# Kernel optimization log

Measured on AMD Instinct MI355X. Metric: run time of the kernel, lower is better.

The kernel has to match this reference:

```python
import jax, jax.numpy as jnp
import numpy as np
import math

B, H, W = 8, 256, 256
CIN, COUT, K = 64, 64, 3
STYLE_IN = 512  # latent dim fed into EqualLinear
LIN_SCALE = 1.0 / math.sqrt(STYLE_IN)        # EqualLinear scale (lr_mul=1)
CONV_SCALE = 1.0 / math.sqrt(CIN * K * K)    # ModulatedConv2D scale


def setup_inputs() -> dict:
    key = jax.random.key(0)
    k1, k2, k3, k4 = jax.random.split(key, 4)
    inputs = jax.random.normal(k1, (B, H, W, CIN), dtype=jnp.float32)
    style = jax.random.normal(k2, (B, STYLE_IN), dtype=jnp.float32)
    # EqualLinear params: weight ~ N(0,1), bias init = 1
    mod_weight = jax.random.normal(k3, (STYLE_IN, CIN), dtype=jnp.float32)
    mod_bias = jnp.ones((CIN,), dtype=jnp.float32)
    # Conv weight [1, out_channel, in_channel, k, k] ~ N(0,1)
    weight = jax.random.normal(k4, (1, COUT, CIN, K, K), dtype=jnp.float32)
    return {"inputs": inputs, "style": style, "mod_weight": mod_weight,
            "mod_bias": mod_bias, "weight": weight}


def _per_sample_conv(xb, wb):
    # xb: [H, W, Cin]; wb: [Cout, Cin, K, K]
    w_hwio = jnp.transpose(wb, (2, 3, 1, 0))  # [K, K, Cin, Cout]
    y = jax.lax.conv_general_dilated(
        xb[None], w_hwio, window_strides=(1, 1), padding="SAME",
        dimension_numbers=("NHWC", "HWIO", "NHWC"))
    return y[0]


def reference(inputs, style, mod_weight, mod_bias, weight):
    # EqualLinear modulation: s = style @ (W * scale) + bias  -> [B, Cin]
    s = style @ (mod_weight * LIN_SCALE) + mod_bias
    # Modulate: [B, Cout, Cin, K, K]
    w = CONV_SCALE * weight * s[:, None, :, None, None]
    # Demodulate over (Cin, K, K)
    demod = jax.lax.rsqrt(jnp.sum(jnp.square(w), axis=(2, 3, 4)) + 1e-8)
    w = w * demod[:, :, None, None, None]
    # Grouped conv (groups = batch) == per-sample conv, vmapped over batch
    out = jax.vmap(_per_sample_conv)(inputs, w)  # [B, H, W, Cout]
    return out
```

## Files before the change

kernel.cpp:

```cpp
#include <hip/hip_runtime.h>

#define BATCH 8
#define HH 256
#define WW 256
#define CI 64
#define CO 64
#define STYLE_IN 512

typedef __bf16 bf16x8 __attribute__((ext_vector_type(8)));
typedef float  f32x4  __attribute__((ext_vector_type(4)));
typedef unsigned short u16x8 __attribute__((ext_vector_type(8)));

static __device__ inline unsigned short f2bf(float f) {
    union { float f; unsigned int u; } a; a.f = f;
    unsigned int u = a.u;
    u += 0x7fffu + ((u >> 16) & 1u);
    return (unsigned short)(u >> 16);
}

__global__ __launch_bounds__(256) void modulate_kernel(
    const float* __restrict__ style, const float* __restrict__ mod_weight,
    const float* __restrict__ mod_bias, const float* __restrict__ weight,
    unsigned short* __restrict__ wbf)
{
    const int b = blockIdx.x;
    const int t = threadIdx.x;
    __shared__ float sp[4][64];
    __shared__ float s_mod[64];
    __shared__ float dpart[64][4];
    __shared__ float demod[64];

    const float LIN_SCALE  = 0.044194173824159216f;
    const float CONV_SCALE = 0.041666666666666664f;

    {
        const int ci = t & 63, part = t >> 6;
        float acc = 0.f;
        const float* st = style + b * STYLE_IN + part * 128;
        const float* mw = mod_weight + part * 128 * 64 + ci;
        #pragma unroll 8
        for (int j = 0; j < 128; ++j) acc += st[j] * mw[j * 64];
        sp[part][ci] = acc;
    }
    __syncthreads();
    if (t < 64)
        s_mod[t] = (sp[0][t] + sp[1][t] + sp[2][t] + sp[3][t]) * LIN_SCALE + mod_bias[t];
    __syncthreads();

    {
        const int co = t >> 2, part = t & 3;
        float acc = 0.f;
        const float* wp = weight + co * 576 + part * 144;
        #pragma unroll
        for (int ci2 = 0; ci2 < 16; ++ci2) {
            float s = s_mod[part * 16 + ci2];
            #pragma unroll
            for (int tp = 0; tp < 9; ++tp) {
                float v = wp[ci2 * 9 + tp] * s;
                acc += v * v;
            }
        }
        dpart[co][part] = acc * (CONV_SCALE * CONV_SCALE);
    }
    __syncthreads();
    if (t < 64)
        demod[t] = rsqrtf(dpart[t][0] + dpart[t][1] + dpart[t][2] + dpart[t][3] + 1e-8f);
    __syncthreads();

    for (int i = t; i < 9 * 64 * 64; i += 256) {
        int ci  = i & 63;
        int co  = (i >> 6) & 63;
        int tap = i >> 12;
        float v = CONV_SCALE * weight[co * 576 + ci * 9 + tap] * s_mod[ci] * demod[co];
        wbf[((b * 9 + tap) * 64 + co) * 64 + ci] = f2bf(v);
    }
}

#define PXS 72
#define ROWPX 130
#define ROW_ELEMS (ROWPX * PXS)

__global__ __launch_bounds__(256, 2) void conv_kernel(
    const float* __restrict__ x, const unsigned short* __restrict__ wbf,
    float* __restrict__ out)
{
    __shared__ unsigned short xs[4 * ROW_ELEMS];

    const int tid = threadIdx.x;
    const int x0  = blockIdx.x * 128;
    const int y0  = blockIdx.y * 8;
    const int b   = blockIdx.z;

    auto issue = [&](int yin, f32x4* v) {
        const bool rok = (unsigned)yin < (unsigned)HH;
        const float* src = x + ((size_t)(b * HH + (rok ? yin : 0))) * WW * CI;
        #pragma unroll
        for (int k = 0; k < 5; ++k) {
            int i  = tid + k * 256;
            int px = i >> 3, cg = i & 7;
            int xin = x0 - 1 + px;
            bool ok = rok && ((unsigned)xin < (unsigned)WW) && (i < 1040);
            const float* p = src + (size_t)xin * CI + cg * 8;
            f32x4 z = {0.f, 0.f, 0.f, 0.f};
            v[2 * k]     = ok ? *(const f32x4*)p       : z;
            v[2 * k + 1] = ok ? *(const f32x4*)(p + 4) : z;
        }
    };
    auto commit = [&](int slot, const f32x4* v) {
        unsigned short* dst = xs + slot * ROW_ELEMS;
        #pragma unroll
        for (int k = 0; k < 5; ++k) {
            int i = tid + k * 256;
            if (k == 4 && i >= 1040) continue;
            int px = i >> 3, cg = i & 7;
            u16x8 u;
            #pragma unroll
            for (int e = 0; e < 4; ++e) {
                u[e]     = f2bf(v[2 * k][e]);
                u[e + 4] = f2bf(v[2 * k + 1][e]);
            }
            *(u16x8*)&dst[px * PXS + cg * 8] = u;
        }
    };

    {
        f32x4 v[10];
        issue(y0 - 1, v); commit(0, v);
        issue(y0,     v); commit(1, v);
        issue(y0 + 1, v); commit(2, v);
    }

    const int wave = tid >> 6, lane = tid & 63;
    const int lm = lane & 15, lq = lane >> 4;
    const int wr = wave >> 1;
    const int wc = wave & 1;
    const int p0 = wr * 64;

    bf16x8 wreg[9][2][2];
    {
        const unsigned short* wl = wbf + (size_t)b * 9 * 4096
                                 + (size_t)(wc * 32 + lm) * 64 + lq * 8;
        #pragma unroll
        for (int tap = 0; tap < 9; ++tap)
            #pragma unroll
            for (int ni = 0; ni < 2; ++ni)
                #pragma unroll
                for (int ks = 0; ks < 2; ++ks)
                    wreg[tap][ni][ks] =
                        *(const bf16x8*)(wl + tap * 4096 + ni * 1024 + ks * 32);
    }

    __syncthreads();

    const int aoff_lane = (p0 + lm) * PXS + lq * 8;

    f32x4 vbuf[10];
    issue(y0 + 2, vbuf);

    #pragma unroll
    for (int j = 0; j < 8; ++j) {
        const int y = y0 + j;

        f32x4 acc[4][2];
        #pragma unroll
        for (int mi = 0; mi < 4; ++mi)
            #pragma unroll
            for (int ni = 0; ni < 2; ++ni)
                acc[mi][ni] = (f32x4){0.f, 0.f, 0.f, 0.f};

        const unsigned short* bases[3] = {
            xs + ((y)     & 3) * ROW_ELEMS,
            xs + ((y + 1) & 3) * ROW_ELEMS,
            xs + ((y + 2) & 3) * ROW_ELEMS,
        };

        #pragma unroll
        for (int kh = 0; kh < 3; ++kh) {
            const unsigned short* bs = bases[kh] + aoff_lane;
            #pragma unroll
            for (int kw = 0; kw < 3; ++kw) {
                #pragma unroll
                for (int ks = 0; ks < 2; ++ks) {
                    #pragma unroll
                    for (int mi = 0; mi < 4; ++mi) {
                        bf16x8 xf = *(const bf16x8*)(bs + (mi * 16 + kw) * PXS + ks * 32);
                        acc[mi][0] = __builtin_amdgcn_mfma_f32_16x16x32_bf16(
                            wreg[kh * 3 + kw][0][ks], xf, acc[mi][0], 0, 0, 0);
                        acc[mi][1] = __builtin_amdgcn_mfma_f32_16x16x32_bf16(
                            wreg[kh * 3 + kw][1][ks], xf, acc[mi][1], 0, 0, 0);
                    }
                }
            }
        }

        commit((y + 3) & 3, vbuf);

        __syncthreads();

        if (j < 7) issue(y + 3, vbuf);

        float* op = out + ((size_t)(b * HH + y) * WW + x0) * CO;
        #pragma unroll
        for (int mi = 0; mi < 4; ++mi) {
            int pix = p0 + mi * 16 + lm;
            #pragma unroll
            for (int ni = 0; ni < 2; ++ni)
                __builtin_nontemporal_store(acc[mi][ni],
                    (f32x4*)(op + (size_t)pix * CO + wc * 32 + ni * 16 + lq * 4));
        }
    }
}

extern "C" void kernel_launch(void* const* d_in, const int* in_sizes, int n_in,
                              void* d_out, int out_size, void* d_ws, size_t ws_size,
                              hipStream_t stream) {
    const float* inputs     = (const float*)d_in[0];
    const float* style      = (const float*)d_in[1];
    const float* mod_weight = (const float*)d_in[2];
    const float* mod_bias   = (const float*)d_in[3];
    const float* weight     = (const float*)d_in[4];
    float* out = (float*)d_out;
    unsigned short* wbf = (unsigned short*)d_ws;

    modulate_kernel<<<BATCH, 256, 0, stream>>>(style, mod_weight, mod_bias, weight, wbf);
    conv_kernel<<<dim3(2, 32, BATCH), 256, 0, stream>>>(inputs, wbf, out);
}
```

Measured before the change: 300.6 us.

## Split modulation across output-channel groups and pin conv weights in registers

The modulation kernel now launches 8 blocks per batch, each handling 8 output channels, instead of one block per batch doing all 64. This spreads the small weight-prep step over more CUs. In the conv kernel, the weight fragments are loaded as raw u16 vectors and pinned with an empty asm barrier so they stay resident in VGPRs. The row loop is also no longer unrolled, which cuts code size and register pressure but adds loop overhead and may lose some scheduling freedom.

```diff
diff --git a/kernel.cpp b/kernel.cpp
--- a/kernel.cpp
+++ b/kernel.cpp
@@ -18,17 +18,22 @@
     return (unsigned short)(u >> 16);
 }
 
+static __device__ inline bf16x8 as_bf(u16x8 v) {
+    union { u16x8 u; bf16x8 b; } c; c.u = v; return c.b;
+}
+
 __global__ __launch_bounds__(256) void modulate_kernel(
     const float* __restrict__ style, const float* __restrict__ mod_weight,
     const float* __restrict__ mod_bias, const float* __restrict__ weight,
     unsigned short* __restrict__ wbf)
 {
-    const int b = blockIdx.x;
-    const int t = threadIdx.x;
+    const int b   = blockIdx.x;
+    const int oct = blockIdx.y;
+    const int t   = threadIdx.x;
     __shared__ float sp[4][64];
     __shared__ float s_mod[64];
-    __shared__ float dpart[64][4];
-    __shared__ float demod[64];
+    __shared__ float dpart[8][32];
+    __shared__ float demod[8];
 
     const float LIN_SCALE  = 0.044194173824159216f;
     const float CONV_SCALE = 0.041666666666666664f;
@@ -48,31 +53,36 @@
     __syncthreads();
 
     {
-        const int co = t >> 2, part = t & 3;
+        const int col = t >> 5, part = t & 31;
         float acc = 0.f;
-        const float* wp = weight + co * 576 + part * 144;
-        #pragma unroll
-        for (int ci2 = 0; ci2 < 16; ++ci2) {
-            float s = s_mod[part * 16 + ci2];
+        const float* wp = weight + (oct * 8 + col) * 576 + part * 18;
+        #pragma unroll
+        for (int ci2 = 0; ci2 < 2; ++ci2) {
+            float s = s_mod[part * 2 + ci2];
             #pragma unroll
             for (int tp = 0; tp < 9; ++tp) {
                 float v = wp[ci2 * 9 + tp] * s;
                 acc += v * v;
             }
         }
-        dpart[co][part] = acc * (CONV_SCALE * CONV_SCALE);
-    }
-    __syncthreads();
-    if (t < 64)
-        demod[t] = rsqrtf(dpart[t][0] + dpart[t][1] + dpart[t][2] + dpart[t][3] + 1e-8f);
-    __syncthreads();
-
-    for (int i = t; i < 9 * 64 * 64; i += 256) {
+        dpart[col][part] = acc * (CONV_SCALE * CONV_SCALE);
+    }
+    __syncthreads();
+    if (t < 8) {
+        float s = 0.f;
+        #pragma unroll
+        for (int p = 0; p < 32; ++p) s += dpart[t][p];
+        demod[t] = rsqrtf(s + 1e-8f);
+    }
+    __syncthreads();
+
+    for (int i = t; i < 4608; i += 256) {
         int ci  = i & 63;
-        int co  = (i >> 6) & 63;
-        int tap = i >> 12;
-        float v = CONV_SCALE * weight[co * 576 + ci * 9 + tap] * s_mod[ci] * demod[co];
-        wbf[((b * 9 + tap) * 64 + co) * 64 + ci] = f2bf(v);
+        int col = (i >> 6) & 7;
+        int tap = i >> 9;
+        float v = CONV_SCALE * weight[(oct * 8 + col) * 576 + ci * 9 + tap]
+                * s_mod[ci] * demod[col];
+        wbf[((b * 9 + tap) * 64 + oct * 8 + col) * 64 + ci] = f2bf(v);
     }
 }
 
@@ -136,7 +146,7 @@
     const int wc = wave & 1;
     const int p0 = wr * 64;
 
-    bf16x8 wreg[9][2][2];
+    u16x8 wreg[9][2][2];
     {
         const unsigned short* wl = wbf + (size_t)b * 9 * 4096
                                  + (size_t)(wc * 32 + lm) * 64 + lq * 8;
@@ -147,8 +157,15 @@
                 #pragma unroll
                 for (int ks = 0; ks < 2; ++ks)
                     wreg[tap][ni][ks] =
-                        *(const bf16x8*)(wl + tap * 4096 + ni * 1024 + ks * 32);
-    }
+                        *(const u16x8*)(wl + tap * 4096 + ni * 1024 + ks * 32);
+    }
+    #pragma unroll
+    for (int tap = 0; tap < 9; ++tap)
+        #pragma unroll
+        for (int ni = 0; ni < 2; ++ni)
+            #pragma unroll
+            for (int ks = 0; ks < 2; ++ks)
+                asm volatile("" : "+v"(wreg[tap][ni][ks]));
 
     __syncthreads();
 
@@ -157,7 +174,7 @@
     f32x4 vbuf[10];
     issue(y0 + 2, vbuf);
 
-    #pragma unroll
+    #pragma unroll 1
     for (int j = 0; j < 8; ++j) {
         const int y = y0 + j;
 
@@ -185,9 +202,9 @@
                     for (int mi = 0; mi < 4; ++mi) {
                         bf16x8 xf = *(const bf16x8*)(bs + (mi * 16 + kw) * PXS + ks * 32);
                         acc[mi][0] = __builtin_amdgcn_mfma_f32_16x16x32_bf16(
-                            wreg[kh * 3 + kw][0][ks], xf, acc[mi][0], 0, 0, 0);
+                            as_bf(wreg[kh * 3 + kw][0][ks]), xf, acc[mi][0], 0, 0, 0);
                         acc[mi][1] = __builtin_amdgcn_mfma_f32_16x16x32_bf16(
-                            wreg[kh * 3 + kw][1][ks], xf, acc[mi][1], 0, 0, 0);
+                            as_bf(wreg[kh * 3 + kw][1][ks]), xf, acc[mi][1], 0, 0, 0);
                     }
                 }
             }
@@ -222,6 +239,6 @@
     float* out = (float*)d_out;
     unsigned short* wbf = (unsigned short*)d_ws;
 
-    modulate_kernel<<<BATCH, 256, 0, stream>>>(style, mod_weight, mod_bias, weight, wbf);
+    modulate_kernel<<<dim3(BATCH, 8), 256, 0, stream>>>(style, mod_weight, mod_bias, weight, wbf);
     conv_kernel<<<dim3(2, 32, BATCH), 256, 0, stream>>>(inputs, wbf, out);
 }
```

Result: faster. 277.7 us (-7.6%).
